# Kernel optimization log

Measured on AMD Instinct MI355X. Metric: run time of the kernel, lower is better.

Reference implementation:

```python
import jax, jax.numpy as jnp
import numpy as np

N_NODES = 40000
N_EDGES = 320000
N_GRAPHS = 64
IN_DIM = 128
HID4 = 256   # hidden_dim * 4
OUT_DIM = 128
LN_EPS = 1e-5


def setup_inputs() -> dict:
    key = jax.random.key(0)
    ks = jax.random.split(key, 12)
    x = jax.random.normal(ks[0], (N_NODES, IN_DIM), dtype=jnp.float32)
    w = jax.random.uniform(ks[1], (N_EDGES, 4), dtype=jnp.float32)
    src = jax.random.randint(ks[2], (N_EDGES,), 0, N_NODES, dtype=jnp.int32)
    dst = jax.random.randint(ks[3], (N_EDGES,), 0, N_NODES, dtype=jnp.int32)
    graph_ids = jnp.sort(jax.random.randint(ks[4], (N_NODES,), 0, N_GRAPHS, dtype=jnp.int32))
    # parameters (no biases on GraphConv / fc1 linear)
    W1 = jax.random.normal(ks[5], (IN_DIM, HID4), dtype=jnp.float32) / np.sqrt(IN_DIM)
    fc1_W = jax.random.normal(ks[6], (IN_DIM, HID4), dtype=jnp.float32) / np.sqrt(IN_DIM)
    ln_gamma = jnp.ones((HID4,), dtype=jnp.float32)
    ln_beta = jnp.zeros((HID4,), dtype=jnp.float32)
    W2 = jax.random.normal(ks[7], (2 * HID4, HID4), dtype=jnp.float32) / np.sqrt(2 * HID4)
    W3 = jax.random.normal(ks[8], (HID4, OUT_DIM), dtype=jnp.float32) / np.sqrt(HID4)
    return {"x": x, "w": w, "W1": W1, "fc1_W": fc1_W, "ln_gamma": ln_gamma,
            "ln_beta": ln_beta, "W2": W2, "W3": W3,
            "src": src, "dst": dst, "graph_ids": graph_ids}


def _graph_conv(feat, src, dst, ew, W, out_inv_sqrt, in_inv_sqrt):
    # DGL GraphConv, norm='both', bias=False, with scalar edge_weight:
    # h = D_out^{-1/2} x ; m_e = w_e * h[src] ; agg = scatter_add(m, dst) ;
    # out = (D_in^{-1/2} agg) @ W
    h = feat * out_inv_sqrt[:, None]
    m = h[src] * ew[:, None]                       # [E, D] messages
    agg = jax.ops.segment_sum(m, dst, num_segments=N_NODES)
    return (agg * in_inv_sqrt[:, None]) @ W


def reference(x, w, W1, fc1_W, ln_gamma, ln_beta, W2, W3, src, dst, graph_ids):
    # unweighted degree normalization (DGL uses structural degrees, clamp(min=1))
    ones_e = jnp.ones((N_EDGES,), dtype=x.dtype)
    out_deg = jnp.maximum(jax.ops.segment_sum(ones_e, src, num_segments=N_NODES), 1.0)
    in_deg = jnp.maximum(jax.ops.segment_sum(ones_e, dst, num_segments=N_NODES), 1.0)
    out_inv = out_deg ** -0.5
    in_inv = in_deg ** -0.5

    ew = jnp.max(w, axis=1)                        # [E]

    x1 = jax.nn.relu(_graph_conv(x, src, dst, ew, W1, out_inv, in_inv))

    # fc1: Linear(no bias) -> LayerNorm(affine) -> ReLU
    f1 = x @ fc1_W
    mu = jnp.mean(f1, axis=-1, keepdims=True)
    var = jnp.mean((f1 - mu) ** 2, axis=-1, keepdims=True)
    f1 = (f1 - mu) * jax.lax.rsqrt(var + LN_EPS) * ln_gamma + ln_beta
    f1 = jax.nn.relu(f1)

    x1f1 = jnp.concatenate([x1, f1], axis=1)       # [N, 512]
    x2 = jax.nn.relu(_graph_conv(x1f1, src, dst, ew, W2, out_inv, in_inv))
    x3 = jax.nn.relu(_graph_conv(x2, src, dst, ew, W3, out_inv, in_inv))

    # dgl.sum_nodes over batched graph, then row-wise L2 normalize
    readout = jax.ops.segment_sum(x3, graph_ids, num_segments=N_GRAPHS)  # [G, OUT_DIM]
    norm = jnp.maximum(jnp.linalg.norm(readout, axis=1, keepdims=True), 1e-12)
    return readout / norm
```

## Files before the change

### kernel.cpp

```cpp
#include <hip/hip_runtime.h>

#define N_NODES 40000
#define M_PAD   40064
#define N_EDGES 320000
#define N_GRAPHS 64
#define IN_DIM 128
#define HID4 256
#define OUT_DIM 128
#define LN_EPS 1e-5f

typedef short  s16x8  __attribute__((ext_vector_type(8)));
typedef __bf16 bf16x8 __attribute__((ext_vector_type(8)));
typedef float  f32x4  __attribute__((ext_vector_type(4)));

__device__ __forceinline__ unsigned short f2b(float f) {
    unsigned int u = __builtin_bit_cast(unsigned int, f);
    u += 0x7fffu + ((u >> 16) & 1u);
    return (unsigned short)(u >> 16);
}
__device__ __forceinline__ float b2f(unsigned short h) {
    unsigned int u = (unsigned int)h << 16;
    return __builtin_bit_cast(float, u);
}

__device__ __forceinline__ void gll16(const unsigned short* g, short* lds_base) {
    __builtin_amdgcn_global_load_lds(
        (const __attribute__((address_space(1))) unsigned int*)g,
        (__attribute__((address_space(3))) unsigned int*)lds_base, 16, 0, 0);
}


#define XN (N_NODES * IN_DIM)
#define WN 229376
#define PREP_TOT (XN + WN + N_EDGES)

__global__ void prep_all(const float* __restrict__ x, const float* __restrict__ W1,
                         const float* __restrict__ fc1, const float* __restrict__ W2,
                         const float* __restrict__ W3, const float* __restrict__ w,
                         const int* __restrict__ src, const int* __restrict__ dst,
                         unsigned short* __restrict__ xb, unsigned short* __restrict__ W1t,
                         unsigned short* __restrict__ fc1t, unsigned short* __restrict__ W2t,
                         unsigned short* __restrict__ W3t, float* __restrict__ ew,
                         int* __restrict__ cnt_out, int* __restrict__ cnt_in) {
    int idx = blockIdx.x * 256 + threadIdx.x;
    if (idx < XN) { xb[idx] = f2b(x[idx]); return; }
    int j = idx - XN;
    if (j < 32768) { int k = j >> 8, n = j & 255; W1t[n * 128 + k] = f2b(W1[j]); return; }
    j -= 32768;
    if (j < 32768) { int k = j >> 8, n = j & 255; fc1t[n * 128 + k] = f2b(fc1[j]); return; }
    j -= 32768;
    if (j < 131072) { int k = j >> 8, n = j & 255; W2t[n * 512 + k] = f2b(W2[j]); return; }
    j -= 131072;
    if (j < 32768) { int k = j >> 7, n = j & 127; W3t[n * 256 + k] = f2b(W3[j]); return; }
    j -= 32768;
    if (j < N_EDGES) {
        float4 v = ((const float4*)w)[j];
        ew[j] = fmaxf(fmaxf(v.x, v.y), fmaxf(v.z, v.w));
        atomicAdd(&cnt_out[src[j]], 1);
        atomicAdd(&cnt_in[dst[j]], 1);
    }
}

__global__ void scan_part(const int* __restrict__ cnt, int* __restrict__ partial) {
    int b = blockIdx.x;
    int s = 0;
    for (int i = threadIdx.x; i < 1000; i += 256) s += cnt[b * 1000 + i];
#pragma unroll
    for (int m = 1; m < 64; m <<= 1) s += __shfl_xor(s, m);
    __shared__ int wsm[4];
    if ((threadIdx.x & 63) == 0) wsm[threadIdx.x >> 6] = s;
    __syncthreads();
    if (threadIdx.x == 0) partial[b] = wsm[0] + wsm[1] + wsm[2] + wsm[3];
}

__global__ void scan_final(const int* __restrict__ cnt_in, const int* __restrict__ cnt_out,
                           const int* __restrict__ partial, int* __restrict__ off,
                           float* __restrict__ out_inv, float* __restrict__ in_inv) {
    int b = blockIdx.x, tid = threadIdx.x;
    int lane = tid & 63, wv = tid >> 6;
    int pre = 0;
    for (int j = 0; j < b; ++j) pre += partial[j];
    int i = b * 1000 + tid;
    int v = (tid < 1000) ? cnt_in[i] : 0;
    int x = v;
#pragma unroll
    for (int ofs = 1; ofs < 64; ofs <<= 1) {
        int t = __shfl_up(x, ofs);
        if (lane >= ofs) x += t;
    }
    __shared__ int wsum[16];
    if (lane == 63) wsum[wv] = x;
    __syncthreads();
    if (wv == 0 && lane < 16) {
        int s = wsum[lane];
#pragma unroll
        for (int ofs = 1; ofs < 16; ofs <<= 1) {
            int t = __shfl_up(s, ofs);
            if (lane >= ofs) s += t;
        }
        wsum[lane] = s;
    }
    __syncthreads();
    int incl = pre + (wv > 0 ? wsum[wv - 1] : 0) + x;
    if (tid < 1000) {
        off[i] = incl - v;
        in_inv[i] = rsqrtf(fmaxf((float)v, 1.0f));
        out_inv[i] = rsqrtf(fmaxf((float)cnt_out[i], 1.0f));
    }
    if (b == 39 && tid == 999) off[N_NODES] = incl;
}

__global__ void csr_fill(const int* __restrict__ src, const int* __restrict__ dst,
                         const float* __restrict__ ew, const float* __restrict__ out_inv,
                         const int* __restrict__ off, int* __restrict__ cnt_in,
                         int2* __restrict__ es1, int2* __restrict__ es23) {
    int e = blockIdx.x * 256 + threadIdx.x;
    if (e >= N_EDGES) return;
    int d = dst[e];
    int slot = off[d] + atomicSub(&cnt_in[d], 1) - 1;
    int s = src[e];
    float wv = ew[e];
    es1[slot] = make_int2(s, __float_as_int(wv * out_inv[s]));
    es23[slot] = make_int2(s, __float_as_int(wv));
}


template <int D, int RELU>
__global__ void gather_nodes(const unsigned short* __restrict__ h, const int* __restrict__ off,
                             const int2* __restrict__ eg, const float* __restrict__ scale,
                             unsigned short* __restrict__ outb) {
    int n = blockIdx.x;
    int t = threadIdx.x;
    int b = off[n], e = off[n + 1];
    const unsigned int* hu = (const unsigned int*)h;
    float a0 = 0.0f, a1 = 0.0f;
    int i = b;
    for (; i + 3 < e; i += 4) {
        int2 e0 = eg[i], e1 = eg[i + 1], e2 = eg[i + 2], e3 = eg[i + 3];
        unsigned int p0 = hu[(size_t)e0.x * (D / 2) + t];
        unsigned int p1 = hu[(size_t)e1.x * (D / 2) + t];
        unsigned int p2 = hu[(size_t)e2.x * (D / 2) + t];
        unsigned int p3 = hu[(size_t)e3.x * (D / 2) + t];
        float w0 = __int_as_float(e0.y), w1 = __int_as_float(e1.y);
        float w2 = __int_as_float(e2.y), w3 = __int_as_float(e3.y);
        a0 += w0 * b2f((unsigned short)p0) + w1 * b2f((unsigned short)p1)
            + w2 * b2f((unsigned short)p2) + w3 * b2f((unsigned short)p3);
        a1 += w0 * b2f((unsigned short)(p0 >> 16)) + w1 * b2f((unsigned short)(p1 >> 16))
            + w2 * b2f((unsigned short)(p2 >> 16)) + w3 * b2f((unsigned short)(p3 >> 16));
    }
    for (; i < e; ++i) {
        int2 ee = eg[i];
        unsigned int p = hu[(size_t)ee.x * (D / 2) + t];
        float w0 = __int_as_float(ee.y);
        a0 += w0 * b2f((unsigned short)p);
        a1 += w0 * b2f((unsigned short)(p >> 16));
    }
    float sc = scale[n];
    a0 *= sc; a1 *= sc;
    if (RELU) { a0 = fmaxf(a0, 0.0f); a1 = fmaxf(a1, 0.0f); }
    unsigned int o = (unsigned int)f2b(a0) | ((unsigned int)f2b(a1) << 16);
    ((unsigned int*)outb)[(size_t)n * (D / 2) + t] = o;
}


#define G3_NPB 8

__global__ void gather3_ro(const unsigned short* __restrict__ h, const int* __restrict__ off,
                           const int2* __restrict__ eg, const float* __restrict__ scale,
                           const int* __restrict__ gid, float* __restrict__ ro) {
    int t = threadIdx.x;
    int n0 = blockIdx.x * G3_NPB;
    int n1 = n0 + G3_NPB;
    if (n1 > N_NODES) n1 = N_NODES;
    const unsigned int* hu = (const unsigned int*)h;
    float r0 = 0.0f, r1 = 0.0f;
    int cur = gid[n0];
    for (int n = n0; n < n1; ++n) {
        int g = gid[n];
        if (g != cur) {
            atomicAdd(&ro[cur * OUT_DIM + 2 * t], r0);
            atomicAdd(&ro[cur * OUT_DIM + 2 * t + 1], r1);
            r0 = r1 = 0.0f;
            cur = g;
        }
        int b = off[n], e = off[n + 1];
        float a0 = 0.0f, a1 = 0.0f;
        int i = b;
        for (; i + 3 < e; i += 4) {
            int2 e0 = eg[i], e1 = eg[i + 1], e2 = eg[i + 2], e3 = eg[i + 3];
            unsigned int p0 = hu[(size_t)e0.x * 64 + t];
            unsigned int p1 = hu[(size_t)e1.x * 64 + t];
            unsigned int p2 = hu[(size_t)e2.x * 64 + t];
            unsigned int p3 = hu[(size_t)e3.x * 64 + t];
            float w0 = __int_as_float(e0.y), w1 = __int_as_float(e1.y);
            float w2 = __int_as_float(e2.y), w3 = __int_as_float(e3.y);
            a0 += w0 * b2f((unsigned short)p0) + w1 * b2f((unsigned short)p1)
                + w2 * b2f((unsigned short)p2) + w3 * b2f((unsigned short)p3);
            a1 += w0 * b2f((unsigned short)(p0 >> 16)) + w1 * b2f((unsigned short)(p1 >> 16))
                + w2 * b2f((unsigned short)(p2 >> 16)) + w3 * b2f((unsigned short)(p3 >> 16));
        }
        for (; i < e; ++i) {
            int2 ee = eg[i];
            unsigned int p = hu[(size_t)ee.x * 64 + t];
            float w0 = __int_as_float(ee.y);
            a0 += w0 * b2f((unsigned short)p);
            a1 += w0 * b2f((unsigned short)(p >> 16));
        }
        float sc = scale[n];
        r0 += fmaxf(a0 * sc, 0.0f);
        r1 += fmaxf(a1 * sc, 0.0f);
    }
    atomicAdd(&ro[cur * OUT_DIM + 2 * t], r0);
    atomicAdd(&ro[cur * OUT_DIM + 2 * t + 1], r1);
}


__device__ __forceinline__ void gemm_core(short* As, short* Bs,
    const unsigned short* __restrict__ A, const unsigned short* __restrict__ A2,
    const unsigned short* __restrict__ Bt, unsigned short* __restrict__ C,
    const float* __restrict__ rowScaleC, int K1, int K2, int N,
    int relu, int scaleC, int m0, int n0) {
    int tid = threadIdx.x;
    int lane = tid & 63, wave = tid >> 6;
    int wm = (wave >> 1) * 64, wn = (wave & 1) * 64;
    int quad = lane >> 4, r16 = lane & 15;
    const int K = K1 + K2;
    f32x4 acc[4][4] = {};
    int lrow = wave * 16 + (lane >> 2);
    int kc = (lane & 3) * 8;
    short* ldsA = As + wave * 512;
    short* ldsB = Bs + wave * 512;

    for (int k0 = 0; k0 < K; k0 += 32) {
        int kk = k0 + kc;
#pragma unroll
        for (int h = 0; h < 2; ++h) {
            int r = h * 64 + lrow;
            const unsigned short* Ap = (kk < K1)
                ? A  + (size_t)(m0 + r) * K1 + kk
                : A2 + (size_t)(m0 + r) * K2 + (kk - K1);
            gll16(Ap, ldsA + h * 2048);
            gll16(Bt + (size_t)(n0 + r) * K + kk, ldsB + h * 2048);
        }
        __syncthreads();
        s16x8 af[4], bfr[4];
#pragma unroll
        for (int i = 0; i < 4; ++i)
            af[i] = *(const s16x8*)(As + (wm + i * 16 + r16) * 32 + quad * 8);
#pragma unroll
        for (int j = 0; j < 4; ++j)
            bfr[j] = *(const s16x8*)(Bs + (wn + j * 16 + r16) * 32 + quad * 8);
#pragma unroll
        for (int i = 0; i < 4; ++i)
#pragma unroll
            for (int j = 0; j < 4; ++j)
                acc[i][j] = __builtin_amdgcn_mfma_f32_16x16x32_bf16(
                    __builtin_bit_cast(bf16x8, af[i]), __builtin_bit_cast(bf16x8, bfr[j]),
                    acc[i][j], 0, 0, 0);
        __syncthreads();
    }

#pragma unroll
    for (int i = 0; i < 4; ++i) {
        int mbase = m0 + wm + i * 16 + quad * 4;
#pragma unroll
        for (int r = 0; r < 4; ++r) {
            int m = mbase + r;
            float sc = scaleC ? rowScaleC[m] : 1.0f;
#pragma unroll
            for (int j = 0; j < 4; ++j) {
                float v = acc[i][j][r] * sc;
                if (relu) v = fmaxf(v, 0.0f);
                C[(size_t)m * N + n0 + wn + j * 16 + r16] = f2b(v);
            }
        }
    }
}

template <int RELU, int SCALE_C>
__global__ __launch_bounds__(256) void gemm_mfma(
    const unsigned short* __restrict__ A, const unsigned short* __restrict__ A2,
    const unsigned short* __restrict__ Bt, unsigned short* __restrict__ C,
    const float* __restrict__ rowScaleC, int K1, int K2, int N) {
    __shared__ short As[4096];
    __shared__ short Bs[4096];
    gemm_core(As, Bs, A, A2, Bt, C, rowScaleC, K1, K2, N, RELU, SCALE_C,
              blockIdx.x * 128, blockIdx.y * 128);
}


__global__ __launch_bounds__(512) void gemm_dual(
    const unsigned short* __restrict__ A0, const unsigned short* __restrict__ B0,
    unsigned short* __restrict__ C0,
    const unsigned short* __restrict__ A1, const unsigned short* __restrict__ B1,
    unsigned short* __restrict__ C1,
    const float* __restrict__ gamma, const float* __restrict__ beta) {
    __shared__ short As[4096];
    __shared__ short Bs[8192];
    __shared__ float lns[128][4];
    __shared__ float lnq[128][4];
    const unsigned short* A  = blockIdx.z ? A1 : A0;
    const unsigned short* Bt = blockIdx.z ? B1 : B0;
    unsigned short* C        = blockIdx.z ? C1 : C0;
    int tid = threadIdx.x;
    int lane = tid & 63, wave = tid >> 6;
    int wm = (wave >> 2) * 64, wn = (wave & 3) * 64;
    int quad = lane >> 4, r16 = lane & 15;
    int m0 = blockIdx.x * 128;
    f32x4 acc[4][4] = {};
    int lrow = lane >> 2;
    int kc = (lane & 3) * 8;
    short* ldsA = As + wave * 512;
    short* ldsB = Bs + wave * 512;

    for (int k0 = 0; k0 < 128; k0 += 32) {
        int kk = k0 + kc;
        int rr = wave * 16 + lrow;
        gll16(A + (size_t)(m0 + rr) * 128 + kk, ldsA);
        gll16(Bt + (size_t)rr * 128 + kk, ldsB);
        gll16(Bt + (size_t)(128 + rr) * 128 + kk, ldsB + 4096);
        __syncthreads();
        s16x8 af[4], bfr[4];
#pragma unroll
        for (int i = 0; i < 4; ++i)
            af[i] = *(const s16x8*)(As + (wm + i * 16 + r16) * 32 + quad * 8);
#pragma unroll
        for (int j = 0; j < 4; ++j)
            bfr[j] = *(const s16x8*)(Bs + (wn + j * 16 + r16) * 32 + quad * 8);
#pragma unroll
        for (int i = 0; i < 4; ++i)
#pragma unroll
            for (int j = 0; j < 4; ++j)
                acc[i][j] = __builtin_amdgcn_mfma_f32_16x16x32_bf16(
                    __builtin_bit_cast(bf16x8, af[i]), __builtin_bit_cast(bf16x8, bfr[j]),
                    acc[i][j], 0, 0, 0);
        __syncthreads();
    }

    if (blockIdx.z == 0) {
#pragma unroll
        for (int i = 0; i < 4; ++i) {
            int mbase = m0 + wm + i * 16 + quad * 4;
#pragma unroll
            for (int r = 0; r < 4; ++r) {
                int m = mbase + r;
#pragma unroll
                for (int j = 0; j < 4; ++j)
                    C[(size_t)m * 256 + wn + j * 16 + r16] = f2b(fmaxf(acc[i][j][r], 0.0f));
            }
        }
    } else {
#pragma unroll
        for (int i = 0; i < 4; ++i)
#pragma unroll
            for (int r = 0; r < 4; ++r) {
                float s = 0.0f, q = 0.0f;
#pragma unroll
                for (int j = 0; j < 4; ++j) { float v = acc[i][j][r]; s += v; q += v * v; }
#pragma unroll
                for (int m = 1; m < 16; m <<= 1) { s += __shfl_xor(s, m); q += __shfl_xor(q, m); }
                if (r16 == 0) {
                    int row = wm + i * 16 + quad * 4 + r;
                    lns[row][wave & 3] = s;
                    lnq[row][wave & 3] = q;
                }
            }
        __syncthreads();
#pragma unroll
        for (int i = 0; i < 4; ++i) {
#pragma unroll
            for (int r = 0; r < 4; ++r) {
                int row = wm + i * 16 + quad * 4 + r;
                float s = lns[row][0] + lns[row][1] + lns[row][2] + lns[row][3];
                float q = lnq[row][0] + lnq[row][1] + lnq[row][2] + lnq[row][3];
                float mu = s * (1.0f / HID4);
                float var = q * (1.0f / HID4) - mu * mu;
                float rs = rsqrtf(var + LN_EPS);
                int m = m0 + row;
#pragma unroll
                for (int j = 0; j < 4; ++j) {
                    int col = wn + j * 16 + r16;
                    float v = (acc[i][j][r] - mu) * rs * gamma[col] + beta[col];
                    C[(size_t)m * 256 + col] = f2b(fmaxf(v, 0.0f));
                }
            }
        }
    }
}


__global__ void normalize_out(const float* __restrict__ ro, float* __restrict__ out) {
    int g = blockIdx.x;
    int d = threadIdx.x;
    float v = ro[g * OUT_DIM + d];
    float ss = v * v;
#pragma unroll
    for (int m = 1; m < 64; m <<= 1) ss += __shfl_xor(ss, m);
    __shared__ float s2[2];
    if ((d & 63) == 0) s2[d >> 6] = ss;
    __syncthreads();
    float tot = s2[0] + s2[1];
    float norm = fmaxf(sqrtf(tot), 1e-12f);
    out[g * OUT_DIM + d] = v / norm;
}


extern "C" void kernel_launch(void* const* d_in, const int* in_sizes, int n_in,
                              void* d_out, int out_size, void* d_ws, size_t ws_size,
                              hipStream_t stream) {
    const float* x    = (const float*)d_in[0];
    const float* w    = (const float*)d_in[1];
    const float* W1   = (const float*)d_in[2];
    const float* fc1W = (const float*)d_in[3];
    const float* gam  = (const float*)d_in[4];
    const float* bet  = (const float*)d_in[5];
    const float* W2   = (const float*)d_in[6];
    const float* W3   = (const float*)d_in[7];
    const int* src = (const int*)d_in[8];
    const int* dst = (const int*)d_in[9];
    const int* gid = (const int*)d_in[10];
    float* out = (float*)d_out;

    float* ws = (float*)d_ws;
    float* out_inv = ws + 0;
    float* in_inv  = ws + 40000;
    float* ew      = ws + 80000;
    int*   cnt_out = (int*)(ws + 400000);
    int*   cnt_in  = (int*)(ws + 440000);
    float* ro      = ws + 480000;
    unsigned short* W1t  = (unsigned short*)(ws + 488192);
    unsigned short* fc1t = (unsigned short*)(ws + 504576);
    unsigned short* W2t  = (unsigned short*)(ws + 520960);
    unsigned short* W3t  = (unsigned short*)(ws + 586496);
    int*   partial = (int*)(ws + 602880);
    int*   off     = (int*)(ws + 602920);
    int2*  es1     = (int2*)(ws + 642922);
    int2*  es23    = (int2*)(ws + 1282922);
    unsigned short* xb    = (unsigned short*)(ws + 1923000);
    unsigned short* Q3b   = xb;
    unsigned short* agg1b = (unsigned short*)(ws + 4487100);
    unsigned short* x2b   = agg1b;
    unsigned short* x1b   = (unsigned short*)(ws + 9615300);
    unsigned short* f1b   = (unsigned short*)(ws + 14743500);
    unsigned short* P2b   = (unsigned short*)(ws + 19871700);

    hipMemsetAsync(cnt_out, 0, (2 * 40000 + N_GRAPHS * OUT_DIM) * sizeof(float), stream);

    prep_all<<<(PREP_TOT + 255) / 256, 256, 0, stream>>>(x, W1, fc1W, W2, W3, w, src, dst,
                                                         xb, W1t, fc1t, W2t, W3t, ew,
                                                         cnt_out, cnt_in);
    scan_part<<<40, 256, 0, stream>>>(cnt_in, partial);
    scan_final<<<40, 1024, 0, stream>>>(cnt_in, cnt_out, partial, off, out_inv, in_inv);
    csr_fill<<<(N_EDGES + 255) / 256, 256, 0, stream>>>(src, dst, ew, out_inv, off, cnt_in,
                                                        es1, es23);

    gather_nodes<IN_DIM, 0><<<N_NODES, IN_DIM / 2, 0, stream>>>(xb, off, es1, in_inv, agg1b);
    {
        dim3 grid(M_PAD / 128, 1, 2);
        gemm_dual<<<grid, 512, 0, stream>>>(agg1b, W1t, x1b, xb, fc1t, f1b, gam, bet);
    }

    {
        dim3 grid(M_PAD / 128, HID4 / 128);
        gemm_mfma<0, 1><<<grid, 256, 0, stream>>>(x1b, f1b, W2t, P2b, out_inv,
                                                  HID4, HID4, HID4);
    }
    gather_nodes<HID4, 1><<<N_NODES, HID4 / 2, 0, stream>>>(P2b, off, es23, in_inv, x2b);

    {
        dim3 grid(M_PAD / 128, OUT_DIM / 128);
        gemm_mfma<0, 1><<<grid, 256, 0, stream>>>(x2b, nullptr, W3t, Q3b, out_inv,
                                                  HID4, 0, OUT_DIM);
    }
    gather3_ro<<<(N_NODES + G3_NPB - 1) / G3_NPB, 64, 0, stream>>>(Q3b, off, es23, in_inv,
                                                                   gid, ro);
    normalize_out<<<N_GRAPHS, 128, 0, stream>>>(ro, out);
}
```

Before: 285.6 us.

## Fuse scan passes, fold edge-weight max into CSR fill, batch gather nodes, concat layout

Removes the scan_part kernel by having each scan_final block recompute its prefix from cnt_in directly. Moves the edge-weight max from prep_all into csr_fill, which drops the ew buffer. gather_nodes now processes several nodes per block (4 for the first layer, 2 for the second) to cut block count. gemm_dual writes x1 and f1 into one interleaved 512-wide buffer, so the W2 GEMM reads a single contiguous A matrix without a per-tile source branch. The trade-offs are redundant prefix reads in the scan and less parallelism in the gather kernels.

```diff
diff --git a/kernel.cpp b/kernel.cpp
--- a/kernel.cpp
+++ b/kernel.cpp
@@ -36,11 +36,11 @@
 
 __global__ void prep_all(const float* __restrict__ x, const float* __restrict__ W1,
                          const float* __restrict__ fc1, const float* __restrict__ W2,
-                         const float* __restrict__ W3, const float* __restrict__ w,
+                         const float* __restrict__ W3,
                          const int* __restrict__ src, const int* __restrict__ dst,
                          unsigned short* __restrict__ xb, unsigned short* __restrict__ W1t,
                          unsigned short* __restrict__ fc1t, unsigned short* __restrict__ W2t,
-                         unsigned short* __restrict__ W3t, float* __restrict__ ew,
+                         unsigned short* __restrict__ W3t,
                          int* __restrict__ cnt_out, int* __restrict__ cnt_in) {
     int idx = blockIdx.x * 256 + threadIdx.x;
     if (idx < XN) { xb[idx] = f2b(x[idx]); return; }
@@ -54,32 +54,34 @@
     if (j < 32768) { int k = j >> 7, n = j & 127; W3t[n * 256 + k] = f2b(W3[j]); return; }
     j -= 32768;
     if (j < N_EDGES) {
-        float4 v = ((const float4*)w)[j];
-        ew[j] = fmaxf(fmaxf(v.x, v.y), fmaxf(v.z, v.w));
         atomicAdd(&cnt_out[src[j]], 1);
         atomicAdd(&cnt_in[dst[j]], 1);
     }
 }
 
-__global__ void scan_part(const int* __restrict__ cnt, int* __restrict__ partial) {
-    int b = blockIdx.x;
-    int s = 0;
-    for (int i = threadIdx.x; i < 1000; i += 256) s += cnt[b * 1000 + i];
-#pragma unroll
-    for (int m = 1; m < 64; m <<= 1) s += __shfl_xor(s, m);
-    __shared__ int wsm[4];
-    if ((threadIdx.x & 63) == 0) wsm[threadIdx.x >> 6] = s;
-    __syncthreads();
-    if (threadIdx.x == 0) partial[b] = wsm[0] + wsm[1] + wsm[2] + wsm[3];
-}
-
 __global__ void scan_final(const int* __restrict__ cnt_in, const int* __restrict__ cnt_out,
-                           const int* __restrict__ partial, int* __restrict__ off,
+                           int* __restrict__ off,
                            float* __restrict__ out_inv, float* __restrict__ in_inv) {
     int b = blockIdx.x, tid = threadIdx.x;
     int lane = tid & 63, wv = tid >> 6;
-    int pre = 0;
-    for (int j = 0; j < b; ++j) pre += partial[j];
+    __shared__ int red[16];
+    __shared__ int pre_s;
+    int lim = b * 1000;
+    int s = 0;
+    for (int i = tid; i < lim; i += 1024) s += cnt_in[i];
+#pragma unroll
+    for (int m = 1; m < 64; m <<= 1) s += __shfl_xor(s, m);
+    if (lane == 0) red[wv] = s;
+    __syncthreads();
+    if (tid == 0) {
+        int p = 0;
+#pragma unroll
+        for (int k = 0; k < 16; ++k) p += red[k];
+        pre_s = p;
+    }
+    __syncthreads();
+    int pre = pre_s;
+
     int i = b * 1000 + tid;
     int v = (tid < 1000) ? cnt_in[i] : 0;
     int x = v;
@@ -92,13 +94,13 @@
     if (lane == 63) wsum[wv] = x;
     __syncthreads();
     if (wv == 0 && lane < 16) {
-        int s = wsum[lane];
+        int ss = wsum[lane];
 #pragma unroll
         for (int ofs = 1; ofs < 16; ofs <<= 1) {
-            int t = __shfl_up(s, ofs);
-            if (lane >= ofs) s += t;
-        }
-        wsum[lane] = s;
+            int t = __shfl_up(ss, ofs);
+            if (lane >= ofs) ss += t;
+        }
+        wsum[lane] = ss;
     }
     __syncthreads();
     int incl = pre + (wv > 0 ? wsum[wv - 1] : 0) + x;
@@ -111,7 +113,7 @@
 }
 
 __global__ void csr_fill(const int* __restrict__ src, const int* __restrict__ dst,
-                         const float* __restrict__ ew, const float* __restrict__ out_inv,
+                         const float* __restrict__ w, const float* __restrict__ out_inv,
                          const int* __restrict__ off, int* __restrict__ cnt_in,
                          int2* __restrict__ es1, int2* __restrict__ es23) {
     int e = blockIdx.x * 256 + threadIdx.x;
@@ -119,47 +121,52 @@
     int d = dst[e];
     int slot = off[d] + atomicSub(&cnt_in[d], 1) - 1;
     int s = src[e];
-    float wv = ew[e];
+    float4 v = ((const float4*)w)[e];
+    float wv = fmaxf(fmaxf(v.x, v.y), fmaxf(v.z, v.w));
     es1[slot] = make_int2(s, __float_as_int(wv * out_inv[s]));
     es23[slot] = make_int2(s, __float_as_int(wv));
 }
 
 
-template <int D, int RELU>
+template <int D, int RELU, int NPB>
 __global__ void gather_nodes(const unsigned short* __restrict__ h, const int* __restrict__ off,
                              const int2* __restrict__ eg, const float* __restrict__ scale,
                              unsigned short* __restrict__ outb) {
-    int n = blockIdx.x;
     int t = threadIdx.x;
-    int b = off[n], e = off[n + 1];
+    int n0 = blockIdx.x * NPB;
+    int n1 = n0 + NPB;
+    if (n1 > N_NODES) n1 = N_NODES;
     const unsigned int* hu = (const unsigned int*)h;
-    float a0 = 0.0f, a1 = 0.0f;
-    int i = b;
-    for (; i + 3 < e; i += 4) {
-        int2 e0 = eg[i], e1 = eg[i + 1], e2 = eg[i + 2], e3 = eg[i + 3];
-        unsigned int p0 = hu[(size_t)e0.x * (D / 2) + t];
-        unsigned int p1 = hu[(size_t)e1.x * (D / 2) + t];
-        unsigned int p2 = hu[(size_t)e2.x * (D / 2) + t];
-        unsigned int p3 = hu[(size_t)e3.x * (D / 2) + t];
-        float w0 = __int_as_float(e0.y), w1 = __int_as_float(e1.y);
-        float w2 = __int_as_float(e2.y), w3 = __int_as_float(e3.y);
-        a0 += w0 * b2f((unsigned short)p0) + w1 * b2f((unsigned short)p1)
-            + w2 * b2f((unsigned short)p2) + w3 * b2f((unsigned short)p3);
-        a1 += w0 * b2f((unsigned short)(p0 >> 16)) + w1 * b2f((unsigned short)(p1 >> 16))
-            + w2 * b2f((unsigned short)(p2 >> 16)) + w3 * b2f((unsigned short)(p3 >> 16));
-    }
-    for (; i < e; ++i) {
-        int2 ee = eg[i];
-        unsigned int p = hu[(size_t)ee.x * (D / 2) + t];
-        float w0 = __int_as_float(ee.y);
-        a0 += w0 * b2f((unsigned short)p);
-        a1 += w0 * b2f((unsigned short)(p >> 16));
-    }
-    float sc = scale[n];
-    a0 *= sc; a1 *= sc;
-    if (RELU) { a0 = fmaxf(a0, 0.0f); a1 = fmaxf(a1, 0.0f); }
-    unsigned int o = (unsigned int)f2b(a0) | ((unsigned int)f2b(a1) << 16);
-    ((unsigned int*)outb)[(size_t)n * (D / 2) + t] = o;
+    for (int n = n0; n < n1; ++n) {
+        int b = off[n], e = off[n + 1];
+        float a0 = 0.0f, a1 = 0.0f;
+        int i = b;
+        for (; i + 3 < e; i += 4) {
+            int2 e0 = eg[i], e1 = eg[i + 1], e2 = eg[i + 2], e3 = eg[i + 3];
+            unsigned int p0 = hu[(size_t)e0.x * (D / 2) + t];
+            unsigned int p1 = hu[(size_t)e1.x * (D / 2) + t];
+            unsigned int p2 = hu[(size_t)e2.x * (D / 2) + t];
+            unsigned int p3 = hu[(size_t)e3.x * (D / 2) + t];
+            float w0 = __int_as_float(e0.y), w1 = __int_as_float(e1.y);
+            float w2 = __int_as_float(e2.y), w3 = __int_as_float(e3.y);
+            a0 += w0 * b2f((unsigned short)p0) + w1 * b2f((unsigned short)p1)
+                + w2 * b2f((unsigned short)p2) + w3 * b2f((unsigned short)p3);
+            a1 += w0 * b2f((unsigned short)(p0 >> 16)) + w1 * b2f((unsigned short)(p1 >> 16))
+                + w2 * b2f((unsigned short)(p2 >> 16)) + w3 * b2f((unsigned short)(p3 >> 16));
+        }
+        for (; i < e; ++i) {
+            int2 ee = eg[i];
+            unsigned int p = hu[(size_t)ee.x * (D / 2) + t];
+            float w0 = __int_as_float(ee.y);
+            a0 += w0 * b2f((unsigned short)p);
+            a1 += w0 * b2f((unsigned short)(p >> 16));
+        }
+        float sc = scale[n];
+        a0 *= sc; a1 *= sc;
+        if (RELU) { a0 = fmaxf(a0, 0.0f); a1 = fmaxf(a1, 0.0f); }
+        unsigned int o = (unsigned int)f2b(a0) | ((unsigned int)f2b(a1) << 16);
+        ((unsigned int*)outb)[(size_t)n * (D / 2) + t] = o;
+    }
 }
 
 
@@ -216,15 +223,13 @@
 
 
 __device__ __forceinline__ void gemm_core(short* As, short* Bs,
-    const unsigned short* __restrict__ A, const unsigned short* __restrict__ A2,
-    const unsigned short* __restrict__ Bt, unsigned short* __restrict__ C,
-    const float* __restrict__ rowScaleC, int K1, int K2, int N,
-    int relu, int scaleC, int m0, int n0) {
+    const unsigned short* __restrict__ A, const unsigned short* __restrict__ Bt,
+    unsigned short* __restrict__ C, const float* __restrict__ rowScaleC,
+    int K, int N, int relu, int scaleC, int m0, int n0) {
     int tid = threadIdx.x;
     int lane = tid & 63, wave = tid >> 6;
     int wm = (wave >> 1) * 64, wn = (wave & 1) * 64;
     int quad = lane >> 4, r16 = lane & 15;
-    const int K = K1 + K2;
     f32x4 acc[4][4] = {};
     int lrow = wave * 16 + (lane >> 2);
     int kc = (lane & 3) * 8;
@@ -236,10 +241,7 @@
 #pragma unroll
         for (int h = 0; h < 2; ++h) {
             int r = h * 64 + lrow;
-            const unsigned short* Ap = (kk < K1)
-                ? A  + (size_t)(m0 + r) * K1 + kk
-                : A2 + (size_t)(m0 + r) * K2 + (kk - K1);
-            gll16(Ap, ldsA + h * 2048);
+            gll16(A + (size_t)(m0 + r) * K + kk, ldsA + h * 2048);
             gll16(Bt + (size_t)(n0 + r) * K + kk, ldsB + h * 2048);
         }
         __syncthreads();
@@ -279,21 +281,19 @@
 
 template <int RELU, int SCALE_C>
 __global__ __launch_bounds__(256) void gemm_mfma(
-    const unsigned short* __restrict__ A, const unsigned short* __restrict__ A2,
-    const unsigned short* __restrict__ Bt, unsigned short* __restrict__ C,
-    const float* __restrict__ rowScaleC, int K1, int K2, int N) {
+    const unsigned short* __restrict__ A, const unsigned short* __restrict__ Bt,
+    unsigned short* __restrict__ C, const float* __restrict__ rowScaleC, int K, int N) {
     __shared__ short As[4096];
     __shared__ short Bs[4096];
-    gemm_core(As, Bs, A, A2, Bt, C, rowScaleC, K1, K2, N, RELU, SCALE_C,
+    gemm_core(As, Bs, A, Bt, C, rowScaleC, K, N, RELU, SCALE_C,
               blockIdx.x * 128, blockIdx.y * 128);
 }
 
 
 __global__ __launch_bounds__(512) void gemm_dual(
     const unsigned short* __restrict__ A0, const unsigned short* __restrict__ B0,
-    unsigned short* __restrict__ C0,
     const unsigned short* __restrict__ A1, const unsigned short* __restrict__ B1,
-    unsigned short* __restrict__ C1,
+    unsigned short* __restrict__ x1f1,
     const float* __restrict__ gamma, const float* __restrict__ beta) {
     __shared__ short As[4096];
     __shared__ short Bs[8192];
@@ -301,7 +301,7 @@
     __shared__ float lnq[128][4];
     const unsigned short* A  = blockIdx.z ? A1 : A0;
     const unsigned short* Bt = blockIdx.z ? B1 : B0;
-    unsigned short* C        = blockIdx.z ? C1 : C0;
+    unsigned short* C = x1f1 + (blockIdx.z ? 256 : 0);
     int tid = threadIdx.x;
     int lane = tid & 63, wave = tid >> 6;
     int wm = (wave >> 2) * 64, wn = (wave & 3) * 64;
@@ -346,7 +346,7 @@
                 int m = mbase + r;
 #pragma unroll
                 for (int j = 0; j < 4; ++j)
-                    C[(size_t)m * 256 + wn + j * 16 + r16] = f2b(fmaxf(acc[i][j][r], 0.0f));
+                    C[(size_t)m * 512 + wn + j * 16 + r16] = f2b(fmaxf(acc[i][j][r], 0.0f));
             }
         }
     } else {
@@ -381,7 +381,7 @@
                 for (int j = 0; j < 4; ++j) {
                     int col = wn + j * 16 + r16;
                     float v = (acc[i][j][r] - mu) * rs * gamma[col] + beta[col];
-                    C[(size_t)m * 256 + col] = f2b(fmaxf(v, 0.0f));
+                    C[(size_t)m * 512 + col] = f2b(fmaxf(v, 0.0f));
                 }
             }
         }
@@ -424,7 +424,6 @@
     float* ws = (float*)d_ws;
     float* out_inv = ws + 0;
     float* in_inv  = ws + 40000;
-    float* ew      = ws + 80000;
     int*   cnt_out = (int*)(ws + 400000);
     int*   cnt_in  = (int*)(ws + 440000);
     float* ro      = ws + 480000;
@@ -432,7 +431,6 @@
     unsigned short* fc1t = (unsigned short*)(ws + 504576);
     unsigned short* W2t  = (unsigned short*)(ws + 520960);
     unsigned short* W3t  = (unsigned short*)(ws + 586496);
-    int*   partial = (int*)(ws + 602880);
     int*   off     = (int*)(ws + 602920);
     int2*  es1     = (int2*)(ws + 642922);
     int2*  es23    = (int2*)(ws + 1282922);
@@ -440,37 +438,33 @@
     unsigned short* Q3b   = xb;
     unsigned short* agg1b = (unsigned short*)(ws + 4487100);
     unsigned short* x2b   = agg1b;
-    unsigned short* x1b   = (unsigned short*)(ws + 9615300);
-    unsigned short* f1b   = (unsigned short*)(ws + 14743500);
+    unsigned short* x1f1  = (unsigned short*)(ws + 9615300);
     unsigned short* P2b   = (unsigned short*)(ws + 19871700);
 
     hipMemsetAsync(cnt_out, 0, (2 * 40000 + N_GRAPHS * OUT_DIM) * sizeof(float), stream);
 
-    prep_all<<<(PREP_TOT + 255) / 256, 256, 0, stream>>>(x, W1, fc1W, W2, W3, w, src, dst,
-                                                         xb, W1t, fc1t, W2t, W3t, ew,
+    prep_all<<<(PREP_TOT + 255) / 256, 256, 0, stream>>>(x, W1, fc1W, W2, W3, src, dst,
+                                                         xb, W1t, fc1t, W2t, W3t,
                                                          cnt_out, cnt_in);
-    scan_part<<<40, 256, 0, stream>>>(cnt_in, partial);
-    scan_final<<<40, 1024, 0, stream>>>(cnt_in, cnt_out, partial, off, out_inv, in_inv);
-    csr_fill<<<(N_EDGES + 255) / 256, 256, 0, stream>>>(src, dst, ew, out_inv, off, cnt_in,
+    scan_final<<<40, 1024, 0, stream>>>(cnt_in, cnt_out, off, out_inv, in_inv);
+    csr_fill<<<(N_EDGES + 255) / 256, 256, 0, stream>>>(src, dst, w, out_inv, off, cnt_in,
                                                         es1, es23);
 
-    gather_nodes<IN_DIM, 0><<<N_NODES, IN_DIM / 2, 0, stream>>>(xb, off, es1, in_inv, agg1b);
+    gather_nodes<IN_DIM, 0, 4><<<N_NODES / 4, IN_DIM / 2, 0, stream>>>(xb, off, es1, in_inv, agg1b);
     {
         dim3 grid(M_PAD / 128, 1, 2);
-        gemm_dual<<<grid, 512, 0, stream>>>(agg1b, W1t, x1b, xb, fc1t, f1b, gam, bet);
+        gemm_dual<<<grid, 512, 0, stream>>>(agg1b, W1t, xb, fc1t, x1f1, gam, bet);
     }
 
     {
         dim3 grid(M_PAD / 128, HID4 / 128);
-        gemm_mfma<0, 1><<<grid, 256, 0, stream>>>(x1b, f1b, W2t, P2b, out_inv,
-                                                  HID4, HID4, HID4);
-    }
-    gather_nodes<HID4, 1><<<N_NODES, HID4 / 2, 0, stream>>>(P2b, off, es23, in_inv, x2b);
+        gemm_mfma<0, 1><<<grid, 256, 0, stream>>>(x1f1, W2t, P2b, out_inv, 512, HID4);
+    }
+    gather_nodes<HID4, 1, 2><<<N_NODES / 2, HID4 / 2, 0, stream>>>(P2b, off, es23, in_inv, x2b);
 
     {
         dim3 grid(M_PAD / 128, OUT_DIM / 128);
-        gemm_mfma<0, 1><<<grid, 256, 0, stream>>>(x2b, nullptr, W3t, Q3b, out_inv,
-                                                  HID4, 0, OUT_DIM);
+        gemm_mfma<0, 1><<<grid, 256, 0, stream>>>(x2b, W3t, Q3b, out_inv, HID4, OUT_DIM);
     }
     gather3_ro<<<(N_NODES + G3_NPB - 1) / G3_NPB, 64, 0, stream>>>(Q3b, off, es23, in_inv,
                                                                    gid, ro);
```

After: 288.0 us. About the same (+0.8%).
